# Kernel optimization log

Hardware: AMD Instinct MI355X
Metric: run time of the kernel (lower is better)

Reference implementation:

```python
import jax, jax.numpy as jnp
import numpy as np

N, E, D_EMB, D_OUT, K = 4096, 131072, 128, 64, 3


def setup_inputs() -> dict:
    key = jax.random.key(0)
    k1, k2, k3, k4 = jax.random.split(key, 4)
    node_features = jax.random.normal(k1, (N, D_EMB), dtype=jnp.float32)
    edge_index = jax.random.randint(k2, (2, E), 0, N, dtype=jnp.int32)
    edge_weights = jax.random.uniform(k3, (E,), dtype=jnp.float32)
    # xavier_uniform-like init for Emb (shape [embdsize, nin])
    limit = float(np.sqrt(6.0 / (D_EMB + D_OUT)))
    Emb = jax.random.uniform(k4, (D_EMB, D_OUT), dtype=jnp.float32, minval=-limit, maxval=limit)
    return {"node_features": node_features, "Emb": Emb,
            "edge_index": edge_index, "edge_weights": edge_weights}


def reference(node_features, Emb, edge_index, edge_weights):
    # embedding: [N, embdsize] @ [embdsize, nin] -> [N, nin]
    x = node_features @ Emb
    n = x.shape[0]
    A = jnp.zeros((n, n), dtype=x.dtype).at[edge_index[0], edge_index[1]].set(edge_weights)
    # matrix_power(A, K) @ x  ==  K repeated A @ x (associativity), avoids forming A^K
    for _ in range(K):
        x = A @ x
    return x
```

## Files before the change

### kernel.cpp

```cpp
#include <hip/hip_runtime.h>
#include <stdint.h>


#define N_NODES 4096
#define D_EMB   128
#define D_OUT   64

#define CAPN      128
#define CAP_SHIFT 7

__global__ void embed_scatter_kernel(const float* __restrict__ nf,
                                     const float* __restrict__ emb,
                                     float* __restrict__ x,
                                     const int* __restrict__ ei,
                                     const float* __restrict__ ew, int E,
                                     int* __restrict__ cnt,
                                     int4* __restrict__ slots) {
    if (blockIdx.x < 1024) {
        __shared__ float srow[4][D_EMB];
        int wave = threadIdx.x >> 6;
        int lane = threadIdx.x & 63;
        int row  = blockIdx.x * 4 + wave;
        float2 a = ((const float2*)(nf + (size_t)row * D_EMB))[lane];
        srow[wave][2 * lane]     = a.x;
        srow[wave][2 * lane + 1] = a.y;
        __syncthreads();
        float acc = 0.0f;
#pragma unroll 8
        for (int k = 0; k < D_EMB; ++k)
            acc = fmaf(srow[wave][k], emb[k * D_OUT + lane], acc);
        x[row * D_OUT + lane] = acc;
    } else {
        int e = (blockIdx.x - 1024) * blockDim.x + threadIdx.x;
        if (e >= E) return;
        int src = ei[e];
        int dst = ei[E + e];
        int idx = atomicAdd(&cnt[src], 1);
        if (idx < CAPN) {
            int4 s;
            s.x = dst;
            s.y = __float_as_int(ew[e]);
            s.z = e;
            s.w = 0;
            slots[(src << CAP_SHIFT) + idx] = s;
        }
    }
}

__global__ void dedup_spmm_kernel(const int* __restrict__ cnt,
                                  int4* __restrict__ slots,
                                  const float* __restrict__ x,
                                  float* __restrict__ y) {
    __shared__ int   sdst[4][CAPN];
    __shared__ int   seid[4][CAPN];
    __shared__ float sw[4][CAPN];

    int wave = threadIdx.x >> 6;
    int lane = threadIdx.x & 63;
    int row  = blockIdx.x * 4 + wave;
    int c = cnt[row];
    if (c > CAPN) c = CAPN;
    int4* s = slots + ((long)row << CAP_SHIFT);

#pragma unroll
    for (int half = 0; half < 2; ++half) {
        int i = lane + half * 64;
        if (i < c) {
            int4 si = s[i];
            sdst[wave][i] = si.x;
            sw[wave][i]   = __int_as_float(si.y);
            seid[wave][i] = si.z;
        }
    }
    __syncthreads();

#pragma unroll
    for (int half = 0; half < 2; ++half) {
        int i = lane + half * 64;
        if (i < c) {
            int d = sdst[wave][i], id = seid[wave][i];
            bool loser = false;
            for (int j = 0; j < c; ++j)
                loser |= (sdst[wave][j] == d) & (seid[wave][j] > id);
            if (loser) {
                sw[wave][i] = 0.0f;
                ((int*)&s[i])[1] = 0;
            }
        }
    }
    __syncthreads();

    float acc = 0.0f;
    int i = 0;
    for (; i + 8 <= c; i += 8) {
        float vw[8], vx[8];
        int vd[8];
#pragma unroll
        for (int k = 0; k < 8; ++k) vw[k] = sw[wave][i + k];
#pragma unroll
        for (int k = 0; k < 8; ++k) vd[k] = sdst[wave][i + k];
#pragma unroll
        for (int k = 0; k < 8; ++k) vx[k] = x[vd[k] * D_OUT + lane];
#pragma unroll
        for (int k = 0; k < 8; ++k) acc = fmaf(vw[k], vx[k], acc);
    }
    for (; i < c; ++i)
        acc = fmaf(sw[wave][i], x[sdst[wave][i] * D_OUT + lane], acc);
    y[row * D_OUT + lane] = acc;
}

__global__ void spmm_kernel(const int* __restrict__ cnt,
                            const int4* __restrict__ slots,
                            const float* __restrict__ x,
                            float* __restrict__ y) {
    int wave = threadIdx.x >> 6;
    int lane = threadIdx.x & 63;
    int row  = blockIdx.x * 4 + wave;
    int c = cnt[row];
    if (c > CAPN) c = CAPN;
    const int2* s = (const int2*)(slots + ((long)row << CAP_SHIFT));

    float acc = 0.0f;
    int i = 0;
    for (; i + 8 <= c; i += 8) {
        int2 e[8];
#pragma unroll
        for (int k = 0; k < 8; ++k) e[k] = s[2 * (i + k)];
        float vx[8];
#pragma unroll
        for (int k = 0; k < 8; ++k) vx[k] = x[e[k].x * D_OUT + lane];
#pragma unroll
        for (int k = 0; k < 8; ++k)
            acc = fmaf(__int_as_float(e[k].y), vx[k], acc);
    }
    for (; i < c; ++i) {
        int2 ee = s[2 * i];
        acc = fmaf(__int_as_float(ee.y), x[ee.x * D_OUT + lane], acc);
    }
    y[row * D_OUT + lane] = acc;
}

extern "C" void kernel_launch(void* const* d_in, const int* in_sizes, int n_in,
                              void* d_out, int out_size, void* d_ws, size_t ws_size,
                              hipStream_t stream) {
    const float* nf  = (const float*)d_in[0];
    const float* emb = (const float*)d_in[1];
    const int*   ei  = (const int*)d_in[2];
    const float* ew  = (const float*)d_in[3];
    float* out = (float*)d_out;

    const int E = in_sizes[3];

    char* ws = (char*)d_ws;
    size_t o = 0;
    auto take = [&](size_t bytes) -> void* {
        void* p = ws + o;
        o += (bytes + 255) & ~(size_t)255;
        return p;
    };
    int*  cnt   = (int*)take((size_t)N_NODES * 4);
    int4* slots = (int4*)take((size_t)N_NODES * CAPN * 16);
    float* x0   = (float*)take((size_t)N_NODES * D_OUT * 4);
    float* x1   = (float*)take((size_t)N_NODES * D_OUT * 4);

    const int TB = 256;
    const int NB = N_NODES / 4;
    const int SB = (E + TB - 1) / TB;

    hipMemsetAsync(cnt, 0, (size_t)N_NODES * 4, stream);
    embed_scatter_kernel<<<NB + SB, TB, 0, stream>>>(nf, emb, x0,
                                                     ei, ew, E, cnt, slots);
    dedup_spmm_kernel<<<NB, TB, 0, stream>>>(cnt, slots, x0, x1);
    spmm_kernel<<<NB, TB, 0, stream>>>(cnt, slots, x1, x0);
    spmm_kernel<<<NB, TB, 0, stream>>>(cnt, slots, x0, out);
}
```

Measured before the change: 50.70 us.

## Deduplicate edges via per-row open-addressing hash table with atomic max

Replaces the per-row append-with-counter slot list and the O(c^2) duplicate scan with a per-row 128-entry open-addressing hash table. Each edge is packed into 64 bits as (dst+1, edge id, weight), and atomicMax keeps the latest edge id per destination. The SpMM kernels compact non-empty slots with ballot/popcount, so all three passes share one kernel and no separate dedup pass is needed. The cost is a larger memset (4 MB instead of 16 KB), CAS contention during scatter, and every SpMM pass now reads all 128 slots per row.

```diff
diff --git a/kernel.cpp b/kernel.cpp
--- a/kernel.cpp
+++ b/kernel.cpp
@@ -6,16 +6,19 @@
 #define D_EMB   128
 #define D_OUT   64
 
-#define CAPN      128
-#define CAP_SHIFT 7
+#define RSLOTS     128
+#define RS_SHIFT   7
+
+__device__ __forceinline__ uint32_t dhash(uint32_t d) {
+    return (d * 2654435761u) >> 25;
+}
 
 __global__ void embed_scatter_kernel(const float* __restrict__ nf,
                                      const float* __restrict__ emb,
                                      float* __restrict__ x,
                                      const int* __restrict__ ei,
                                      const float* __restrict__ ew, int E,
-                                     int* __restrict__ cnt,
-                                     int4* __restrict__ slots) {
+                                     unsigned long long* __restrict__ slots) {
     if (blockIdx.x < 1024) {
         __shared__ float srow[4][D_EMB];
         int wave = threadIdx.x >> 6;
@@ -35,58 +38,52 @@
         if (e >= E) return;
         int src = ei[e];
         int dst = ei[E + e];
-        int idx = atomicAdd(&cnt[src], 1);
-        if (idx < CAPN) {
-            int4 s;
-            s.x = dst;
-            s.y = __float_as_int(ew[e]);
-            s.z = e;
-            s.w = 0;
-            slots[(src << CAP_SHIFT) + idx] = s;
+        unsigned long long key = (unsigned long long)(dst + 1);
+        unsigned long long entry = (key << 49)
+                                 | ((unsigned long long)(uint32_t)e << 32)
+                                 | (unsigned long long)__float_as_uint(ew[e]);
+        unsigned long long* rs = slots + ((size_t)src << RS_SHIFT);
+        uint32_t h = dhash((uint32_t)dst) & (RSLOTS - 1);
+        while (true) {
+            unsigned long long cur = rs[h];
+            if ((cur >> 49) == key) { atomicMax(&rs[h], entry); break; }
+            if (cur == 0ULL) {
+                unsigned long long old = atomicCAS(&rs[h], 0ULL, entry);
+                if (old == 0ULL) break;
+                if ((old >> 49) == key) { atomicMax(&rs[h], entry); break; }
+            }
+            h = (h + 1) & (RSLOTS - 1);
         }
     }
 }
 
-__global__ void dedup_spmm_kernel(const int* __restrict__ cnt,
-                                  int4* __restrict__ slots,
-                                  const float* __restrict__ x,
-                                  float* __restrict__ y) {
-    __shared__ int   sdst[4][CAPN];
-    __shared__ int   seid[4][CAPN];
-    __shared__ float sw[4][CAPN];
+__global__ void spmm_kernel(const unsigned long long* __restrict__ slots,
+                            const float* __restrict__ x,
+                            float* __restrict__ y) {
+    __shared__ int   sdst[4][RSLOTS];
+    __shared__ float sw[4][RSLOTS];
 
     int wave = threadIdx.x >> 6;
     int lane = threadIdx.x & 63;
     int row  = blockIdx.x * 4 + wave;
-    int c = cnt[row];
-    if (c > CAPN) c = CAPN;
-    int4* s = slots + ((long)row << CAP_SHIFT);
+    const unsigned long long* rs = slots + ((size_t)row << RS_SHIFT);
 
-#pragma unroll
-    for (int half = 0; half < 2; ++half) {
-        int i = lane + half * 64;
-        if (i < c) {
-            int4 si = s[i];
-            sdst[wave][i] = si.x;
-            sw[wave][i]   = __int_as_float(si.y);
-            seid[wave][i] = si.z;
-        }
+    unsigned long long e0 = rs[lane];
+    unsigned long long e1 = rs[lane + 64];
+    unsigned long long m0 = __ballot(e0 != 0ULL);
+    unsigned long long m1 = __ballot(e1 != 0ULL);
+    unsigned long long lt = (1ULL << lane) - 1ULL;
+    int c0 = __popcll(m0);
+    int c  = c0 + __popcll(m1);
+    if (e0) {
+        int p = __popcll(m0 & lt);
+        sdst[wave][p] = (int)(e0 >> 49) - 1;
+        sw[wave][p]   = __uint_as_float((uint32_t)e0);
     }
-    __syncthreads();
-
-#pragma unroll
-    for (int half = 0; half < 2; ++half) {
-        int i = lane + half * 64;
-        if (i < c) {
-            int d = sdst[wave][i], id = seid[wave][i];
-            bool loser = false;
-            for (int j = 0; j < c; ++j)
-                loser |= (sdst[wave][j] == d) & (seid[wave][j] > id);
-            if (loser) {
-                sw[wave][i] = 0.0f;
-                ((int*)&s[i])[1] = 0;
-            }
-        }
+    if (e1) {
+        int p = c0 + __popcll(m1 & lt);
+        sdst[wave][p] = (int)(e1 >> 49) - 1;
+        sw[wave][p]   = __uint_as_float((uint32_t)e1);
     }
     __syncthreads();
 
@@ -109,37 +106,6 @@
     y[row * D_OUT + lane] = acc;
 }
 
-__global__ void spmm_kernel(const int* __restrict__ cnt,
-                            const int4* __restrict__ slots,
-                            const float* __restrict__ x,
-                            float* __restrict__ y) {
-    int wave = threadIdx.x >> 6;
-    int lane = threadIdx.x & 63;
-    int row  = blockIdx.x * 4 + wave;
-    int c = cnt[row];
-    if (c > CAPN) c = CAPN;
-    const int2* s = (const int2*)(slots + ((long)row << CAP_SHIFT));
-
-    float acc = 0.0f;
-    int i = 0;
-    for (; i + 8 <= c; i += 8) {
-        int2 e[8];
-#pragma unroll
-        for (int k = 0; k < 8; ++k) e[k] = s[2 * (i + k)];
-        float vx[8];
-#pragma unroll
-        for (int k = 0; k < 8; ++k) vx[k] = x[e[k].x * D_OUT + lane];
-#pragma unroll
-        for (int k = 0; k < 8; ++k)
-            acc = fmaf(__int_as_float(e[k].y), vx[k], acc);
-    }
-    for (; i < c; ++i) {
-        int2 ee = s[2 * i];
-        acc = fmaf(__int_as_float(ee.y), x[ee.x * D_OUT + lane], acc);
-    }
-    y[row * D_OUT + lane] = acc;
-}
-
 extern "C" void kernel_launch(void* const* d_in, const int* in_sizes, int n_in,
                               void* d_out, int out_size, void* d_ws, size_t ws_size,
                               hipStream_t stream) {
@@ -158,19 +124,19 @@
         o += (bytes + 255) & ~(size_t)255;
         return p;
     };
-    int*  cnt   = (int*)take((size_t)N_NODES * 4);
-    int4* slots = (int4*)take((size_t)N_NODES * CAPN * 16);
-    float* x0   = (float*)take((size_t)N_NODES * D_OUT * 4);
-    float* x1   = (float*)take((size_t)N_NODES * D_OUT * 4);
+    unsigned long long* slots =
+        (unsigned long long*)take((size_t)N_NODES * RSLOTS * 8);
+    float* x0 = (float*)take((size_t)N_NODES * D_OUT * 4);
+    float* x1 = (float*)take((size_t)N_NODES * D_OUT * 4);
 
     const int TB = 256;
     const int NB = N_NODES / 4;
     const int SB = (E + TB - 1) / TB;
 
-    hipMemsetAsync(cnt, 0, (size_t)N_NODES * 4, stream);
+    hipMemsetAsync(slots, 0, (size_t)N_NODES * RSLOTS * 8, stream);
     embed_scatter_kernel<<<NB + SB, TB, 0, stream>>>(nf, emb, x0,
-                                                     ei, ew, E, cnt, slots);
-    dedup_spmm_kernel<<<NB, TB, 0, stream>>>(cnt, slots, x0, x1);
-    spmm_kernel<<<NB, TB, 0, stream>>>(cnt, slots, x1, x0);
-    spmm_kernel<<<NB, TB, 0, stream>>>(cnt, slots, x0, out);
+                                                     ei, ew, E, slots);
+    spmm_kernel<<<NB, TB, 0, stream>>>(slots, x0, x1);
+    spmm_kernel<<<NB, TB, 0, stream>>>(slots, x1, x0);
+    spmm_kernel<<<NB, TB, 0, stream>>>(slots, x0, out);
 }
```

Result: faster. 46.67 us (-7.9%).
